# Kernel tuning notes

Measured on AMD Instinct MI355X. Metric: run time of the kernel, lower is better.

Reference implementation:

```python
import jax, jax.numpy as jnp
import numpy as np

EPS = 1e-6
GROUPS = 8


def setup_inputs() -> dict:
    key = jax.random.key(0)
    ks = jax.random.split(key, 8)
    B, C, H, W = 4, 128, 64, 64
    s = 1.0 / np.sqrt(C)
    return {
        "x": jax.random.normal(ks[0], (B, C, H, W), jnp.float32),
        "gn_scale": jnp.ones((C,), jnp.float32),
        "gn_bias": jnp.zeros((C,), jnp.float32),
        "wq": jax.random.normal(ks[1], (C, C), jnp.float32) * s,
        "bq": jnp.zeros((C,), jnp.float32),
        "wk": jax.random.normal(ks[2], (C, C), jnp.float32) * s,
        "bk": jnp.zeros((C,), jnp.float32),
        "wv": jax.random.normal(ks[3], (C, C), jnp.float32) * s,
        "bv": jnp.zeros((C,), jnp.float32),
        "wp": jax.random.normal(ks[4], (C, C), jnp.float32) * s,
        "bp": jnp.zeros((C,), jnp.float32),
    }


def _group_norm(x, scale, bias):
    B, C, H, W = x.shape
    g = x.reshape(B, GROUPS, C // GROUPS, H * W)
    mu = g.mean(axis=(2, 3), keepdims=True)
    var = g.var(axis=(2, 3), keepdims=True)
    g = (g - mu) * jax.lax.rsqrt(var + EPS)
    g = g.reshape(B, C, H, W)
    return g * scale[None, :, None, None] + bias[None, :, None, None]


def reference(x, gn_scale, gn_bias, wq, bq, wk, bk, wv, bv, wp, bp):
    B, C, H, W = x.shape
    N = H * W
    h = _group_norm(x, gn_scale, gn_bias).reshape(B, C, N)
    # 1x1 convs == channel matmuls: (C_out, C_in) x (B, C_in, N)
    q = jnp.einsum('oc,bcn->bon', wq, h) + bq[None, :, None]
    k = jnp.einsum('oc,bcn->bon', wk, h) + bk[None, :, None]
    v = jnp.einsum('oc,bcn->bon', wv, h) + bv[None, :, None]
    # scores: (B, N, N), w[b,n,m] = sum_c q[b,c,n] k[b,c,m]
    w = jnp.einsum('bcn,bcm->bnm', q, k) * (C ** -0.5)
    w = jax.nn.softmax(w, axis=-1)
    # h_[b,c,n] = sum_m w[b,n,m] v[b,c,m]
    h_ = jnp.einsum('bnm,bcm->bcn', w, v)
    out = jnp.einsum('oc,bcn->bon', wp, h_) + bp[None, :, None]
    return x + out.reshape(B, C, H, W)
```

## Files before the change

### kernel.cpp

```cpp
#include <hip/hip_runtime.h>
#include <math.h>

#define B_ 4
#define C_ 128
#define N_ 4096
#define NSPLIT 4
#define MT 32
#define PLD 40
#define HLD 136
#define VTLD 24

typedef float floatx4 __attribute__((ext_vector_type(4)));
typedef short bf16x8 __attribute__((ext_vector_type(8)));

__device__ __forceinline__ ushort f2bf(float f) {
  unsigned u = __float_as_uint(f);
  return (ushort)((u + 0x7FFF + ((u >> 16) & 1)) >> 16);
}
__device__ __forceinline__ float bf2f(ushort u) {
  return __uint_as_float(((unsigned)u) << 16);
}
__device__ __forceinline__ unsigned pkbf(float a, float b) {
  return __builtin_amdgcn_perm(__float_as_uint(a) + 0x8000u,
                               __float_as_uint(b) + 0x8000u, 0x07060302u);
}
__device__ __forceinline__ void gl2lds16(const ushort* g, ushort* l) {
  __builtin_amdgcn_global_load_lds(
      (const __attribute__((address_space(1))) void*)g,
      (__attribute__((address_space(3))) void*)l, 16, 0, 0);
}

__global__ __launch_bounds__(256) void prep_kernel(
    const float* __restrict__ x, float* __restrict__ gstat,
    const float* __restrict__ wq, const float* __restrict__ wk,
    const float* __restrict__ wv, const float* __restrict__ wp,
    ushort* __restrict__ wB) {
  if (blockIdx.x >= 256) {
    int i = (blockIdx.x - 256) * 256 + threadIdx.x;
    int m = i >> 14, j = i & 16383;
    const float* src = (m == 0) ? wq : (m == 1) ? wk : (m == 2) ? wv : wp;
    wB[i] = f2bf(src[j]);
    return;
  }
  int b = blockIdx.x >> 6, g = (blockIdx.x >> 3) & 7, part = blockIdx.x & 7;
  const float4* xp = (const float4*)(x + (size_t)(b * C_ + g * 16) * N_) + part * 2048;
  float s = 0.f, ss = 0.f;
  for (int i = threadIdx.x; i < 2048; i += 256) {
    float4 v = xp[i];
    s += v.x + v.y + v.z + v.w;
    ss += v.x * v.x + v.y * v.y + v.z * v.z + v.w * v.w;
  }
  #pragma unroll
  for (int o = 32; o > 0; o >>= 1) {
    s += __shfl_down(s, o, 64);
    ss += __shfl_down(ss, o, 64);
  }
  __shared__ float rs[4], rss[4];
  int wid = threadIdx.x >> 6, lane = threadIdx.x & 63;
  if (lane == 0) { rs[wid] = s; rss[wid] = ss; }
  __syncthreads();
  if (threadIdx.x == 0) {
    int slot = (b * 8 + g) * 8 + part;
    gstat[slot]       = rs[0] + rs[1] + rs[2] + rs[3];
    gstat[256 + slot] = rss[0] + rss[1] + rss[2] + rss[3];
  }
}

__global__ __launch_bounds__(256) void gnqkv_kernel(
    const float* __restrict__ x, const float* __restrict__ gstat,
    const float* __restrict__ scale, const float* __restrict__ bias,
    const ushort* __restrict__ wB,
    const float* __restrict__ bq, const float* __restrict__ bk,
    const float* __restrict__ bv,
    ushort* __restrict__ qT, ushort* __restrict__ kT, ushort* __restrict__ vB) {
  __shared__ __align__(16) ushort hs[16][HLD];
  __shared__ __align__(16) ushort Qt[16][HLD];
  __shared__ __align__(16) ushort Kt[16][HLD];
  __shared__ __align__(16) ushort Vt[128][VTLD];
  __shared__ float sSc[C_], sBi[C_];
  int tid = threadIdx.x;
  int b = blockIdx.x >> 8;
  int n0 = (blockIdx.x & 255) * 16;
  if (tid < 128) {
    int g = tid >> 4;
    float S = 0.f, SS = 0.f;
    #pragma unroll
    for (int p = 0; p < 8; ++p) {
      S  += gstat[(b * 8 + g) * 8 + p];
      SS += gstat[256 + (b * 8 + g) * 8 + p];
    }
    float mu = S * (1.f / 65536.f);
    float var = SS * (1.f / 65536.f) - mu * mu;
    float rstd = rsqrtf(var + 1e-6f);
    float sc = scale[tid] * rstd;
    sSc[tid] = sc;
    sBi[tid] = bias[tid] - mu * sc;
  }
  __syncthreads();
  #pragma unroll
  for (int k2 = 0; k2 < 2; ++k2) {
    int i = tid + k2 * 256;
    int c = i >> 2, n4 = i & 3;
    float4 v = *(const float4*)(x + (size_t)(b * C_ + c) * N_ + n0 + n4 * 4);
    float sc = sSc[c], bi = sBi[c];
    hs[n4 * 4 + 0][c] = f2bf(v.x * sc + bi);
    hs[n4 * 4 + 1][c] = f2bf(v.y * sc + bi);
    hs[n4 * 4 + 2][c] = f2bf(v.z * sc + bi);
    hs[n4 * 4 + 3][c] = f2bf(v.w * sc + bi);
  }
  __syncthreads();
  int lane = tid & 63, w = tid >> 6;
  int col = lane & 15, quad = lane >> 4;
  int oh = w * 32;
  bf16x8 hf[4];
  #pragma unroll
  for (int kc = 0; kc < 4; ++kc)
    hf[kc] = *(const bf16x8*)&hs[col][kc * 32 + quad * 8];
  const ushort* Wq = wB;
  const ushort* Wk = wB + 16384;
  const ushort* Wv = wB + 32768;
  const float scl = 0.12751879752224991f;
  #pragma unroll
  for (int ot = 0; ot < 2; ++ot) {
    int o0 = oh + ot * 16;
    floatx4 aq = (floatx4)0.f, ak = (floatx4)0.f, av = (floatx4)0.f;
    #pragma unroll
    for (int kc = 0; kc < 4; ++kc) {
      int wo = (o0 + col) * C_ + kc * 32 + quad * 8;
      aq = __builtin_amdgcn_mfma_f32_16x16x32_bf16(*(const bf16x8*)&Wq[wo], hf[kc], aq, 0, 0, 0);
      ak = __builtin_amdgcn_mfma_f32_16x16x32_bf16(*(const bf16x8*)&Wk[wo], hf[kc], ak, 0, 0, 0);
      av = __builtin_amdgcn_mfma_f32_16x16x32_bf16(*(const bf16x8*)&Wv[wo], hf[kc], av, 0, 0, 0);
    }
    float4 bqv = *(const float4*)&bq[o0 + quad * 4];
    float4 bkv = *(const float4*)&bk[o0 + quad * 4];
    float4 bvv = *(const float4*)&bv[o0 + quad * 4];
    uint2 qs = { pkbf((aq[1] + bqv.y) * scl, (aq[0] + bqv.x) * scl),
                 pkbf((aq[3] + bqv.w) * scl, (aq[2] + bqv.z) * scl) };
    uint2 ks = { pkbf(ak[1] + bkv.y, ak[0] + bkv.x),
                 pkbf(ak[3] + bkv.w, ak[2] + bkv.z) };
    *(uint2*)&Qt[col][o0 + quad * 4] = qs;
    *(uint2*)&Kt[col][o0 + quad * 4] = ks;
    float vv[4] = {av[0] + bvv.x, av[1] + bvv.y, av[2] + bvv.z, av[3] + bvv.w};
    #pragma unroll
    for (int r = 0; r < 4; ++r)
      Vt[o0 + quad * 4 + r][col] = f2bf(vv[r]);
  }
  __syncthreads();
  {
    int row = tid >> 4, seg = tid & 15;
    size_t dst = ((size_t)b * N_ + n0 + row) * C_ + seg * 8;
    *(uint4*)(qT + dst) = *(const uint4*)&Qt[row][seg * 8];
    *(uint4*)(kT + dst) = *(const uint4*)&Kt[row][seg * 8];
  }
  {
    int o = tid >> 1, seg = tid & 1;
    *(uint4*)(vB + ((size_t)b * C_ + o) * N_ + n0 + seg * 8) = *(const uint4*)&Vt[o][seg * 8];
  }
}

__global__ __launch_bounds__(512, 4) void attn_kernel(
    const ushort* __restrict__ qT, const ushort* __restrict__ kT,
    const ushort* __restrict__ vB, ushort* __restrict__ Op,
    float* __restrict__ Lv) {
  __shared__ __align__(16) ushort Ks[2][MT * 128];
  __shared__ __align__(16) ushort Vs[2][C_ * MT];
  __shared__ __align__(16) ushort Ps[128 * PLD];
  __shared__ float lpart[8][2][16];
  int sp = blockIdx.x & 3;
  int qblk = (blockIdx.x >> 2) & 31;
  int b = blockIdx.x >> 7;
  int n0 = qblk * 128;
  int tid = threadIdx.x, lane = tid & 63, w = tid >> 6;
  int col = lane & 15, quad = lane >> 4;
  int wu = __builtin_amdgcn_readfirstlane(w);
  int mtw = w & 1, qg = w >> 1;
  int qh = w & 1, cq = w >> 1;
  const ushort* kTb = kT + (size_t)b * N_ * C_;
  const ushort* vBb = vB + (size_t)b * C_ * N_;

  bf16x8 qf[2][4];
  #pragma unroll
  for (int qt = 0; qt < 2; ++qt)
    #pragma unroll
    for (int kc = 0; kc < 4; ++kc)
      qf[qt][kc] = *(const bf16x8*)(qT + ((size_t)b * N_ + n0 + qg * 32 + qt * 16 + col) * C_ + kc * 32 + quad * 8);

  floatx4 Oacc[4][2];
  #pragma unroll
  for (int qt = 0; qt < 4; ++qt)
    #pragma unroll
    for (int ct = 0; ct < 2; ++ct) Oacc[qt][ct] = (floatx4)0.f;
  float lacc[2] = {0.f, 0.f};

  #define STAGE(m0v, buf)                                                            \
    {                                                                                \
      int r = wu * 4 + (lane >> 4);                                                  \
      int pos = (lane & 15) ^ (r & 7);                                               \
      gl2lds16(kTb + (size_t)((m0v) + r) * 128 + pos * 8, &Ks[buf][wu * 512]);       \
      int c = wu * 16 + (lane >> 2);                                                 \
      gl2lds16(vBb + (size_t)c * N_ + (m0v) + (lane & 3) * 8, &Vs[buf][wu * 512]);   \
    }

  STAGE(sp * 1024, 0);
  __syncthreads();

  for (int it = 0; it < 1024 / MT; ++it) {
    if (it < 1024 / MT - 1) STAGE(sp * 1024 + (it + 1) * MT, (it + 1) & 1);
    const ushort* KsB = Ks[it & 1];
    const ushort* VsB = Vs[it & 1];

    floatx4 st[2];
    {
      int row = mtw * 16 + col;
      bf16x8 kf[4];
      #pragma unroll
      for (int kc = 0; kc < 4; ++kc)
        kf[kc] = *(const bf16x8*)&KsB[row * 128 + (((4 * kc + quad) ^ (col & 7)) * 8)];
      #pragma unroll
      for (int qt = 0; qt < 2; ++qt) {
        floatx4 acc = (floatx4)0.f;
        #pragma unroll
        for (int kc = 0; kc < 4; ++kc)
          acc = __builtin_amdgcn_mfma_f32_16x16x32_bf16(kf[kc], qf[qt][kc], acc, 0, 0, 0);
        st[qt] = acc;
      }
    }
    #pragma unroll
    for (int qt = 0; qt < 2; ++qt) {
      int prow = (qg * 32 + qt * 16 + col) * PLD + mtw * 16;
      float p0 = exp2f(st[qt][0]);
      float p1 = exp2f(st[qt][1]);
      float p2 = exp2f(st[qt][2]);
      float p3 = exp2f(st[qt][3]);
      uint2 pk = { pkbf(p1, p0), pkbf(p3, p2) };
      *(uint2*)&Ps[prow + quad * 4] = pk;
      lacc[qt] += (p0 + p1) + (p2 + p3);
    }
    __syncthreads();
    bf16x8 vf[2];
    #pragma unroll
    for (int ct = 0; ct < 2; ++ct)
      vf[ct] = *(const bf16x8*)&VsB[(cq * 32 + ct * 16 + col) * MT + quad * 8];
    #pragma unroll
    for (int qt = 0; qt < 4; ++qt) {
      bf16x8 pf = *(const bf16x8*)&Ps[(qh * 64 + qt * 16 + col) * PLD + quad * 8];
      #pragma unroll
      for (int ct = 0; ct < 2; ++ct)
        Oacc[qt][ct] = __builtin_amdgcn_mfma_f32_16x16x32_bf16(pf, vf[ct], Oacc[qt][ct], 0, 0, 0);
    }
    __syncthreads();
  }

  ushort* OpB = Op + (((size_t)sp * B_ + b) * N_ + n0) * C_;
  #pragma unroll
  for (int qt = 0; qt < 4; ++qt)
    #pragma unroll
    for (int ct = 0; ct < 2; ++ct)
      #pragma unroll
      for (int r = 0; r < 4; ++r)
        OpB[(size_t)(qh * 64 + qt * 16 + quad * 4 + r) * C_ + cq * 32 + ct * 16 + col] =
            f2bf(Oacc[qt][ct][r]);
  #pragma unroll
  for (int qt = 0; qt < 2; ++qt) {
    float lsum = lacc[qt];
    lsum += __shfl_xor(lsum, 16, 64);
    lsum += __shfl_xor(lsum, 32, 64);
    if (quad == 0) lpart[w][qt][col] = lsum;
  }
  __syncthreads();
  if ((w & 1) == 0 && quad == 0) {
    #pragma unroll
    for (int qt = 0; qt < 2; ++qt) {
      int idx = b * N_ + n0 + (w >> 1) * 32 + qt * 16 + col;
      Lv[(size_t)sp * (B_ * N_) + idx] = lpart[w][qt][col] + lpart[w + 1][qt][col];
    }
  }
}

__global__ __launch_bounds__(256) void mergeproj_kernel(
    const ushort* __restrict__ Op, const float* __restrict__ Lv,
    const ushort* __restrict__ wpB, const float* __restrict__ bp,
    const float* __restrict__ x, float* __restrict__ out) {
  __shared__ __align__(16) ushort tile[16 * HLD];
  int tid = threadIdx.x;
  int b = blockIdx.x >> 8;
  int n0 = (blockIdx.x & 255) * 16;
  {
    int n = tid >> 4, cc = tid & 15;
    int nIdx = b * N_ + n0 + n;
    float den = Lv[0 * (B_ * N_) + nIdx] + Lv[1 * (B_ * N_) + nIdx] +
                Lv[2 * (B_ * N_) + nIdx] + Lv[3 * (B_ * N_) + nIdx];
    float inv = 1.f / den;
    float o[8];
    #pragma unroll
    for (int j = 0; j < 8; ++j) o[j] = 0.f;
    #pragma unroll
    for (int sp = 0; sp < NSPLIT; ++sp) {
      uint4 d = *(const uint4*)&Op[((size_t)sp * (B_ * N_) + nIdx) * C_ + cc * 8];
      unsigned dd[4] = {d.x, d.y, d.z, d.w};
      #pragma unroll
      for (int j = 0; j < 4; ++j) {
        o[j * 2]     += bf2f((ushort)(dd[j] & 0xFFFF));
        o[j * 2 + 1] += bf2f((ushort)(dd[j] >> 16));
      }
    }
    uint4 res;
    res.x = pkbf(o[1] * inv, o[0] * inv);
    res.y = pkbf(o[3] * inv, o[2] * inv);
    res.z = pkbf(o[5] * inv, o[4] * inv);
    res.w = pkbf(o[7] * inv, o[6] * inv);
    *(uint4*)&tile[n * HLD + cc * 8] = res;
  }
  __syncthreads();
  int lane = tid & 63, w = tid >> 6;
  int col = lane & 15, quad = lane >> 4;
  int oh = w * 32;
  bf16x8 hf[4];
  #pragma unroll
  for (int kc = 0; kc < 4; ++kc)
    hf[kc] = *(const bf16x8*)&tile[col * HLD + kc * 32 + quad * 8];
  #pragma unroll
  for (int ot = 0; ot < 2; ++ot) {
    int o0 = oh + ot * 16;
    floatx4 acc = (floatx4)0.f;
    #pragma unroll
    for (int kc = 0; kc < 4; ++kc) {
      int wo = (o0 + col) * C_ + kc * 32 + quad * 8;
      acc = __builtin_amdgcn_mfma_f32_16x16x32_bf16(*(const bf16x8*)&wpB[wo], hf[kc], acc, 0, 0, 0);
    }
    float4 bpv = *(const float4*)&bp[o0 + quad * 4];
    float bb[4] = {bpv.x, bpv.y, bpv.z, bpv.w};
    #pragma unroll
    for (int r = 0; r < 4; ++r) {
      size_t idx = ((size_t)b * C_ + o0 + quad * 4 + r) * N_ + n0 + col;
      out[idx] = acc[r] + bb[r] + x[idx];
    }
  }
}

extern "C" void kernel_launch(void* const* d_in, const int* in_sizes, int n_in,
                              void* d_out, int out_size, void* d_ws, size_t ws_size,
                              hipStream_t stream) {
  const float* x        = (const float*)d_in[0];
  const float* gn_scale = (const float*)d_in[1];
  const float* gn_bias  = (const float*)d_in[2];
  const float* wq = (const float*)d_in[3];
  const float* bq = (const float*)d_in[4];
  const float* wk = (const float*)d_in[5];
  const float* bk = (const float*)d_in[6];
  const float* wv = (const float*)d_in[7];
  const float* bv = (const float*)d_in[8];
  const float* wp = (const float*)d_in[9];
  const float* bp = (const float*)d_in[10];
  float* out = (float*)d_out;

  char* ws = (char*)d_ws;
  float*  Lv    = (float*)(ws + 262144);
  ushort* wB    = (ushort*)(ws + 524288);
  float*  gstat = (float*)(ws + 655360);
  ushort* qT    = (ushort*)(ws + (4u << 20));
  ushort* kT    = (ushort*)(ws + (8u << 20));
  ushort* vB    = (ushort*)(ws + (12u << 20));
  ushort* Op    = (ushort*)(ws + (16u << 20));
  ushort* wpB   = wB + 49152;

  prep_kernel<<<512, 256, 0, stream>>>(x, gstat, wq, wk, wv, wp, wB);
  gnqkv_kernel<<<1024, 256, 0, stream>>>(x, gstat, gn_scale, gn_bias, wB, bq, bk, bv, qT, kT, vB);
  attn_kernel<<<512, 512, 0, stream>>>(qT, kT, vB, Op, Lv);
  mergeproj_kernel<<<1024, 256, 0, stream>>>(Op, Lv, wpB, bp, x, out);
}
```

Before: 153.8 us.

## Load K and V fragments directly from global memory, dropping LDS staging

Removes the double-buffered LDS staging of K and V tiles, which used global_load_lds. Each wave now reads its K and V MFMA fragments straight from global memory, relying on L2/L1 caching. The PV matmul is also remapped so each wave covers 32 query rows by 64 channels instead of 64 by 32. This cuts LDS traffic and footprint, but gives up the prefetch overlap and puts global-load latency inside the loop, with no explicit pipelining to hide it.

```diff
diff --git a/kernel.cpp b/kernel.cpp
--- a/kernel.cpp
+++ b/kernel.cpp
@@ -23,11 +23,6 @@
 __device__ __forceinline__ unsigned pkbf(float a, float b) {
   return __builtin_amdgcn_perm(__float_as_uint(a) + 0x8000u,
                                __float_as_uint(b) + 0x8000u, 0x07060302u);
-}
-__device__ __forceinline__ void gl2lds16(const ushort* g, ushort* l) {
-  __builtin_amdgcn_global_load_lds(
-      (const __attribute__((address_space(1))) void*)g,
-      (__attribute__((address_space(3))) void*)l, 16, 0, 0);
 }
 
 __global__ __launch_bounds__(256) void prep_kernel(
@@ -162,8 +157,6 @@
     const ushort* __restrict__ qT, const ushort* __restrict__ kT,
     const ushort* __restrict__ vB, ushort* __restrict__ Op,
     float* __restrict__ Lv) {
-  __shared__ __align__(16) ushort Ks[2][MT * 128];
-  __shared__ __align__(16) ushort Vs[2][C_ * MT];
   __shared__ __align__(16) ushort Ps[128 * PLD];
   __shared__ float lpart[8][2][16];
   int sp = blockIdx.x & 3;
@@ -172,9 +165,8 @@
   int n0 = qblk * 128;
   int tid = threadIdx.x, lane = tid & 63, w = tid >> 6;
   int col = lane & 15, quad = lane >> 4;
-  int wu = __builtin_amdgcn_readfirstlane(w);
   int mtw = w & 1, qg = w >> 1;
-  int qh = w & 1, cq = w >> 1;
+  int qq = w & 3, ch = w >> 2;
   const ushort* kTb = kT + (size_t)b * N_ * C_;
   const ushort* vBb = vB + (size_t)b * C_ * N_;
 
@@ -185,45 +177,29 @@
     for (int kc = 0; kc < 4; ++kc)
       qf[qt][kc] = *(const bf16x8*)(qT + ((size_t)b * N_ + n0 + qg * 32 + qt * 16 + col) * C_ + kc * 32 + quad * 8);
 
-  floatx4 Oacc[4][2];
-  #pragma unroll
-  for (int qt = 0; qt < 4; ++qt)
-    #pragma unroll
-    for (int ct = 0; ct < 2; ++ct) Oacc[qt][ct] = (floatx4)0.f;
+  floatx4 Oacc[2][4];
+  #pragma unroll
+  for (int qt = 0; qt < 2; ++qt)
+    #pragma unroll
+    for (int ct = 0; ct < 4; ++ct) Oacc[qt][ct] = (floatx4)0.f;
   float lacc[2] = {0.f, 0.f};
 
-  #define STAGE(m0v, buf)                                                            \
-    {                                                                                \
-      int r = wu * 4 + (lane >> 4);                                                  \
-      int pos = (lane & 15) ^ (r & 7);                                               \
-      gl2lds16(kTb + (size_t)((m0v) + r) * 128 + pos * 8, &Ks[buf][wu * 512]);       \
-      int c = wu * 16 + (lane >> 2);                                                 \
-      gl2lds16(vBb + (size_t)c * N_ + (m0v) + (lane & 3) * 8, &Vs[buf][wu * 512]);   \
-    }
-
-  STAGE(sp * 1024, 0);
-  __syncthreads();
+  const ushort* kRow = kTb + (size_t)(sp * 1024 + mtw * 16 + col) * C_;
+  const ushort* vRow = vBb + (size_t)(ch * 64 + col) * N_ + sp * 1024;
 
   for (int it = 0; it < 1024 / MT; ++it) {
-    if (it < 1024 / MT - 1) STAGE(sp * 1024 + (it + 1) * MT, (it + 1) & 1);
-    const ushort* KsB = Ks[it & 1];
-    const ushort* VsB = Vs[it & 1];
-
+    bf16x8 kf[4];
+    #pragma unroll
+    for (int kc = 0; kc < 4; ++kc)
+      kf[kc] = *(const bf16x8*)(kRow + (size_t)it * MT * C_ + kc * 32 + quad * 8);
     floatx4 st[2];
-    {
-      int row = mtw * 16 + col;
-      bf16x8 kf[4];
+    #pragma unroll
+    for (int qt = 0; qt < 2; ++qt) {
+      floatx4 acc = (floatx4)0.f;
       #pragma unroll
       for (int kc = 0; kc < 4; ++kc)
-        kf[kc] = *(const bf16x8*)&KsB[row * 128 + (((4 * kc + quad) ^ (col & 7)) * 8)];
-      #pragma unroll
-      for (int qt = 0; qt < 2; ++qt) {
-        floatx4 acc = (floatx4)0.f;
-        #pragma unroll
-        for (int kc = 0; kc < 4; ++kc)
-          acc = __builtin_amdgcn_mfma_f32_16x16x32_bf16(kf[kc], qf[qt][kc], acc, 0, 0, 0);
-        st[qt] = acc;
-      }
+        acc = __builtin_amdgcn_mfma_f32_16x16x32_bf16(kf[kc], qf[qt][kc], acc, 0, 0, 0);
+      st[qt] = acc;
     }
     #pragma unroll
     for (int qt = 0; qt < 2; ++qt) {
@@ -237,28 +213,26 @@
       lacc[qt] += (p0 + p1) + (p2 + p3);
     }
     __syncthreads();
-    bf16x8 vf[2];
-    #pragma unroll
-    for (int ct = 0; ct < 2; ++ct)
-      vf[ct] = *(const bf16x8*)&VsB[(cq * 32 + ct * 16 + col) * MT + quad * 8];
-    #pragma unroll
-    for (int qt = 0; qt < 4; ++qt) {
-      bf16x8 pf = *(const bf16x8*)&Ps[(qh * 64 + qt * 16 + col) * PLD + quad * 8];
+    #pragma unroll
+    for (int qt = 0; qt < 2; ++qt) {
+      bf16x8 pf = *(const bf16x8*)&Ps[(qq * 32 + qt * 16 + col) * PLD + quad * 8];
       #pragma unroll
-      for (int ct = 0; ct < 2; ++ct)
-        Oacc[qt][ct] = __builtin_amdgcn_mfma_f32_16x16x32_bf16(pf, vf[ct], Oacc[qt][ct], 0, 0, 0);
+      for (int ct = 0; ct < 4; ++ct) {
+        bf16x8 vf = *(const bf16x8*)(vRow + (size_t)(ct * 16) * N_ + it * MT + quad * 8);
+        Oacc[qt][ct] = __builtin_amdgcn_mfma_f32_16x16x32_bf16(pf, vf, Oacc[qt][ct], 0, 0, 0);
+      }
     }
     __syncthreads();
   }
 
   ushort* OpB = Op + (((size_t)sp * B_ + b) * N_ + n0) * C_;
   #pragma unroll
-  for (int qt = 0; qt < 4; ++qt)
-    #pragma unroll
-    for (int ct = 0; ct < 2; ++ct)
+  for (int qt = 0; qt < 2; ++qt)
+    #pragma unroll
+    for (int ct = 0; ct < 4; ++ct)
       #pragma unroll
       for (int r = 0; r < 4; ++r)
-        OpB[(size_t)(qh * 64 + qt * 16 + quad * 4 + r) * C_ + cq * 32 + ct * 16 + col] =
+        OpB[(size_t)(qq * 32 + qt * 16 + quad * 4 + r) * C_ + ch * 64 + ct * 16 + col] =
             f2bf(Oacc[qt][ct][r]);
   #pragma unroll
   for (int qt = 0; qt < 2; ++qt) {
```

Result: slower. 228.0 us (+48.2%).
